# Performance work log

Measured on AMD Instinct MI355X. Metric: run time of the kernel, lower is better.

Reference implementation:

```python
import jax, jax.numpy as jnp
import numpy as np

NEG_SLOPE = 0.01  # nn.LeakyReLU default
EPS = 1e-5        # nn.LayerNorm default


def _layernorm(x):
    # parameter-free LayerNorm over last dim (source calls nn.LayerNorm() with no shape)
    mu = jnp.mean(x, axis=-1, keepdims=True)
    var = jnp.var(x, axis=-1, keepdims=True)
    return (x - mu) * jax.lax.rsqrt(var + EPS)


def _leaky_relu(x):
    return jnp.where(x >= 0, x, NEG_SLOPE * x)


def setup_inputs() -> dict:
    key = jax.random.key(0)
    ks = jax.random.split(key, 9)
    B, N, F_IN, F_HID, HEADS, F_OUT = 8, 1024, 384, 96, 8, 384
    s_v = 1.0 / np.sqrt(F_IN)
    s_qk = 1.0 / np.sqrt(F_HID)
    s_m = 1.0 / np.sqrt(F_HID * HEADS + F_IN)
    return {
        "X": jax.random.normal(ks[0], (B, N, F_IN), jnp.float32),
        "Wv": jax.random.uniform(ks[1], (F_IN, F_HID), jnp.float32, -s_v, s_v),
        "bv": jax.random.uniform(ks[2], (F_HID,), jnp.float32, -s_v, s_v),
        "Wq": jax.random.uniform(ks[3], (F_HID, HEADS), jnp.float32, -s_qk, s_qk),
        "bq": jax.random.uniform(ks[4], (HEADS,), jnp.float32, -s_qk, s_qk),
        "Wk": jax.random.uniform(ks[5], (F_HID, HEADS), jnp.float32, -s_qk, s_qk),
        "bk": jax.random.uniform(ks[6], (HEADS,), jnp.float32, -s_qk, s_qk),
        "Wm": jax.random.uniform(ks[7], (F_HID * HEADS + F_IN, F_OUT), jnp.float32, -s_m, s_m),
        "bm": jax.random.uniform(ks[8], (F_OUT,), jnp.float32, -s_m, s_m),
    }


def reference(X, Wv, bv, Wq, bq, Wk, bk, Wm, bm):
    B, N, _ = X.shape
    Hn = _layernorm(X)
    # MultiHeadGraphAtten
    V = Hn @ Wv + bv                      # [B, N, f_hid]
    Q = V @ Wq + bq                       # [B, N, heads]
    K = V @ Wk + bk                       # [B, N, heads]
    A = _leaky_relu(jnp.einsum('bih,bjh->bijh', Q, K))  # [B, N, N, heads]
    A = jax.nn.softmax(A, axis=3)         # softmax over heads (dim=3), faithful to source
    Hh = jnp.einsum('bijh,bjf->bihf', A, V)  # [B, N, heads, f_hid]
    H = Hh.reshape(B, N, -1)              # [B, N, heads*f_hid]
    H = jnp.concatenate([H, X], axis=2)   # residual concat
    O = _layernorm(H) @ Wm + bm
    O = _leaky_relu(O)                    # dropout is identity in eval
    return jnp.concatenate([O, H], axis=2)
```

## Files before the change

kernel.cpp:

```cpp
#include <hip/hip_runtime.h>
#include <hip/hip_bf16.h>
#include <math.h>

#define BB 8
#define NN 1024
#define F_IN 384
#define F_HID 96
#define HEADS 8
#define F_OUT 384
#define ROWS (BB*NN)
#define H_DIM 1152
#define OUT_DIM 1536
#define NEG 0.01f
#define LN_EPS 1e-5f
#define LOG2E 1.4426950408889634f

typedef __bf16 bf16x8 __attribute__((ext_vector_type(8)));
typedef float  f32x4  __attribute__((ext_vector_type(4)));

static __device__ __forceinline__ unsigned short b16u(float x) {
    union { __bf16 h; unsigned short u; } c; c.h = (__bf16)x; return c.u;
}
static __device__ __forceinline__ unsigned int pk2(float lo, float hi) {
    return (unsigned int)b16u(lo) | ((unsigned int)b16u(hi) << 16);
}

typedef __attribute__((address_space(1))) const unsigned char g1_t;
typedef __attribute__((address_space(3))) unsigned char l3_t;
static __device__ __forceinline__ void gl16(const void* g, void* l) {
    __builtin_amdgcn_global_load_lds((g1_t*)g, (l3_t*)l, 16, 0, 0);
}

__global__ __launch_bounds__(256) void kW(const float* __restrict__ Wm,
                                          const float* __restrict__ Wv,
                                          unsigned short* __restrict__ WmT,
                                          unsigned short* __restrict__ WvT) {
    __shared__ float tile[32][33];
    const int t = threadIdx.x;
    const int bid = (int)blockIdx.x;
    const float* src; unsigned short* dst;
    int k0, n0, srcld, dstld;
    if (bid < 432) {
        k0 = (bid / 12) * 32; n0 = (bid % 12) * 32;
        src = Wm; dst = WmT; srcld = F_OUT; dstld = H_DIM;
    } else {
        const int e = bid - 432;
        k0 = (e / 3) * 32; n0 = (e % 3) * 32;
        src = Wv; dst = WvT; srcld = F_HID; dstld = F_IN;
    }
#pragma unroll
    for (int p = 0; p < 4; ++p) {
        const int e = t + 256*p, kk = e >> 5, nn = e & 31;
        tile[kk][nn] = src[(size_t)(k0 + kk) * srcld + n0 + nn];
    }
    __syncthreads();
#pragma unroll
    for (int p = 0; p < 4; ++p) {
        const int e = t + 256*p, nn = e >> 5, kk = e & 31;
        dst[(size_t)(n0 + nn) * dstld + k0 + kk] = b16u(tile[kk][nn]);
    }
}

__global__ __launch_bounds__(384) void kA(const float* __restrict__ X,
                                          const unsigned short* __restrict__ WvT,
                                          const float* __restrict__ bv,
                                          const float* __restrict__ Wq, const float* __restrict__ bq,
                                          const float* __restrict__ Wk, const float* __restrict__ bk,
                                          unsigned short* __restrict__ VT,
                                          float* __restrict__ Qw, float* __restrict__ Kw) {
    __shared__ __align__(16) unsigned short xn[16][392];
    __shared__ float vsh[96][17];
    const int t = threadIdx.x;
    const int bid = (int)blockIdx.x;
    const int swz = (bid & 7) * 64 + (bid >> 3);
    const int i0 = swz * 16;
    const int b = i0 >> 10, i_in = i0 & 1023;
    const int w = t >> 6, l = t & 63, m = l & 15, g = l >> 4;

    if (t < 256) {
        const int r = t >> 4, l16 = t & 15;
        const float4* xrow = (const float4*)(X + (size_t)(i0 + r) * F_IN);
        float4 xv[6];
        float s = 0.f, sq = 0.f;
#pragma unroll
        for (int k = 0; k < 6; ++k) {
            xv[k] = xrow[l16 + 16*k];
            s  += xv[k].x + xv[k].y + xv[k].z + xv[k].w;
            sq += xv[k].x*xv[k].x + xv[k].y*xv[k].y + xv[k].z*xv[k].z + xv[k].w*xv[k].w;
        }
#pragma unroll
        for (int msk = 1; msk < 16; msk <<= 1) { s += __shfl_xor(s, msk); sq += __shfl_xor(sq, msk); }
        const float mu  = s * (1.f/F_IN);
        const float var = sq * (1.f/F_IN) - mu*mu;
        const float rstd = rsqrtf(var + LN_EPS);
#pragma unroll
        for (int k = 0; k < 6; ++k) {
            ushort4 h4;
            h4.x = b16u((xv[k].x - mu) * rstd);
            h4.y = b16u((xv[k].y - mu) * rstd);
            h4.z = b16u((xv[k].z - mu) * rstd);
            h4.w = b16u((xv[k].w - mu) * rstd);
            *(ushort4*)&xn[r][4*(l16 + 16*k)] = h4;
        }
    }
    __syncthreads();

    const f32x4 z4 = {0.f, 0.f, 0.f, 0.f};
    f32x4 acc = z4;
    const unsigned short* Br = WvT + (size_t)(w*16 + m) * F_IN + g*8;
#pragma unroll
    for (int ks = 0; ks < 12; ++ks) {
        const bf16x8 af  = *(const bf16x8*)&xn[m][ks*32 + g*8];
        const bf16x8 bfr = *(const bf16x8*)(Br + ks*32);
        acc = __builtin_amdgcn_mfma_f32_16x16x32_bf16(af, bfr, acc, 0, 0, 0);
    }
    {
        const int f = w*16 + m;
        const float bvv = bv[f];
#pragma unroll
        for (int r = 0; r < 4; ++r)
            vsh[f][g*4 + r] = acc[r] + bvv;
    }
    __syncthreads();

    {
        const int f = t >> 2, ic = (t & 3) * 4;
        ushort4 h4;
        h4.x = b16u(vsh[f][ic]);   h4.y = b16u(vsh[f][ic+1]);
        h4.z = b16u(vsh[f][ic+2]); h4.w = b16u(vsh[f][ic+3]);
        *(ushort4*)&VT[((size_t)b * F_HID + f) * NN + i_in + ic] = h4;
    }

    if (t < 256) {
        const int i_loc = t & 15, h = (t >> 4) & 7;
        const bool isQ = (t < 128);
        const float* Wx = isQ ? Wq : Wk;
        float a = isQ ? bq[h] : bk[h];
#pragma unroll 8
        for (int f = 0; f < F_HID; ++f)
            a = fmaf(vsh[f][i_loc], Wx[f*HEADS + h], a);
        if (isQ) Qw[(size_t)(i0 + i_loc) * HEADS + h] = a;
        else     Kw[(size_t)(i0 + i_loc) * HEADS + h] = a;
    }
}

__global__ __launch_bounds__(512, 4) void kB(const float* __restrict__ X,
                                             const unsigned short* __restrict__ VT,
                                             const float* __restrict__ Qw,
                                             const float* __restrict__ Kw,
                                             float* __restrict__ out,
                                             unsigned short* __restrict__ Hn) {
    __shared__ float q_sh[16][8];
    __shared__ float kT[2][HEADS][64];
    __shared__ __align__(16) unsigned short Wt[2][HEADS][16][64];
    __shared__ __align__(16) unsigned short vt_sh[2][F_HID][64];
    __shared__ float lnS[8][16], lnQ2[8][16];
    __shared__ float sxS[16], sx2S[16];
    __shared__ float mu_sh[16], rs_sh[16];

    const int t = threadIdx.x;
    const int bid = (int)blockIdx.x;
    const int swz = (bid & 7) * 64 + (bid >> 3);
    const int b  = swz >> 6;
    const int i0 = (swz & 63) * 16;
    const int w = t >> 6, l = t & 63, m = l & 15, g = l >> 4;
    const int hp = w >> 1, fh = w & 1;
    const int si = t >> 5, jd = t & 31;

    if (t < 128) ((float*)q_sh)[t] = Qw[((size_t)(b*NN + i0)) * HEADS + t];

    const f32x4 z4 = {0.f, 0.f, 0.f, 0.f};
    f32x4 acc[2][3];
#pragma unroll
    for (int h2 = 0; h2 < 2; ++h2)
#pragma unroll
        for (int fb = 0; fb < 3; ++fb) acc[h2][fb] = z4;

    const size_t vtbase = (size_t)b * F_HID * NN;
    const size_t krow   = (size_t)b * NN;

#define SMAX(kb, db)                                                                   \
    {                                                                                  \
        float2 kk[8];                                                                  \
        _Pragma("unroll")                                                              \
        for (int h = 0; h < 8; ++h)                                                    \
            kk[h] = *(const float2*)&kT[kb][h][2*jd];                                  \
        float p0[8], p1[8];                                                            \
        float s0 = 0.f, s1 = 0.f;                                                      \
        _Pragma("unroll")                                                              \
        for (int h = 0; h < 8; ++h) {                                                  \
            float a0 = q[h] * kk[h].x; a0 = fmaxf(a0, NEG*a0);                         \
            float a1 = q[h] * kk[h].y; a1 = fmaxf(a1, NEG*a1);                         \
            p0[h] = __builtin_amdgcn_exp2f(a0); s0 += p0[h];                           \
            p1[h] = __builtin_amdgcn_exp2f(a1); s1 += p1[h];                           \
        }                                                                              \
        const float inv0 = 1.f / s0, inv1 = 1.f / s1;                                  \
        char* wbase = (char*)Wt + (db)*16384 + si*128                                  \
                    + ((((jd>>2) ^ (si & 7))) << 4) + ((jd & 3) << 2);                 \
        _Pragma("unroll")                                                              \
        for (int h = 0; h < 8; ++h)                                                    \
            *(unsigned int*)(wbase + h*2048) = pk2(p0[h]*inv0, p1[h]*inv1);            \
    }

    {
        uint4 vr0, vr1;
        {
            const int f = t >> 3, u = t & 7;
            vr0 = *(const uint4*)(VT + vtbase + (size_t)f*NN + u*8);
        }
        if (t < 256) {
            const int e = t + 512, f2 = e >> 3, u2 = e & 7;
            vr1 = *(const uint4*)(VT + vtbase + (size_t)f2*NN + u2*8);
        }
        const float ka = Kw[(krow + l) * HEADS + w];
        const float kb_ = Kw[(krow + 64 + l) * HEADS + w];
        {
            const int f = t >> 3, u = t & 7;
            *(uint4*)((char*)vt_sh + f*128 + ((u ^ (f & 7)) << 4)) = vr0;
        }
        if (t < 256) {
            const int e = t + 512, f2 = e >> 3, u2 = e & 7;
            *(uint4*)((char*)vt_sh + f2*128 + ((u2 ^ (f2 & 7)) << 4)) = vr1;
        }
        kT[0][w][l] = ka;
        kT[1][w][l] = kb_;
    }
    __syncthreads();

    float q[8];
#pragma unroll
    for (int h = 0; h < 8; ++h) q[h] = q_sh[si][h] * LOG2E;

    SMAX(0, 0);
    __syncthreads();

    for (int c = 0; c < 16; ++c) {
        const int cur = c & 1, nxt = cur ^ 1;

        uint4 vr0, vr1; float kr = 0.f;
        if (c < 15) {
            const int j0n = (c + 1) * 64;
            {
                const int f = t >> 3, u = t & 7;
                vr0 = *(const uint4*)(VT + vtbase + (size_t)f*NN + j0n + u*8);
            }
            if (t < 256) {
                const int e = t + 512, f2 = e >> 3, u2 = e & 7;
                vr1 = *(const uint4*)(VT + vtbase + (size_t)f2*NN + j0n + u2*8);
            }
        }
        if (c < 14) kr = Kw[(krow + (size_t)(c + 2)*64 + l) * HEADS + w];

        if (c < 15) SMAX(nxt, nxt);

#pragma unroll
        for (int kh = 0; kh < 2; ++kh) {
            const int swzu = ((kh*4 + g) ^ (m & 7)) << 4;
            bf16x8 af[2];
#pragma unroll
            for (int h2 = 0; h2 < 2; ++h2)
                af[h2] = *(const bf16x8*)((const char*)Wt + cur*16384
                                          + (hp*2 + h2)*2048 + m*128 + swzu);
            bf16x8 bfr[3];
#pragma unroll
            for (int fb = 0; fb < 3; ++fb)
                bfr[fb] = *(const bf16x8*)((const char*)vt_sh + cur*12288
                                           + (fh*48 + fb*16 + m)*128 + swzu);
#pragma unroll
            for (int h2 = 0; h2 < 2; ++h2)
#pragma unroll
                for (int fb = 0; fb < 3; ++fb)
                    acc[h2][fb] = __builtin_amdgcn_mfma_f32_16x16x32_bf16(
                        af[h2], bfr[fb], acc[h2][fb], 0, 0, 0);
        }

        if (c < 15) {
            {
                const int f = t >> 3, u = t & 7;
                *(uint4*)((char*)vt_sh + nxt*12288 + f*128 + ((u ^ (f & 7)) << 4)) = vr0;
            }
            if (t < 256) {
                const int e = t + 512, f2 = e >> 3, u2 = e & 7;
                *(uint4*)((char*)vt_sh + nxt*12288 + f2*128 + ((u2 ^ (f2 & 7)) << 4)) = vr1;
            }
        }
        if (c < 14) kT[cur][w][l] = kr;
        __syncthreads();
    }
#undef SMAX

    float s[4] = {0,0,0,0}, s2[4] = {0,0,0,0};
#pragma unroll
    for (int h2 = 0; h2 < 2; ++h2)
#pragma unroll
        for (int fb = 0; fb < 3; ++fb)
#pragma unroll
            for (int r = 0; r < 4; ++r) {
                const float v = acc[h2][fb][r];
                s[r] += v; s2[r] += v*v;
            }
#pragma unroll
    for (int msk = 1; msk < 16; msk <<= 1)
#pragma unroll
        for (int r = 0; r < 4; ++r) {
            s[r]  += __shfl_xor(s[r],  msk);
            s2[r] += __shfl_xor(s2[r], msk);
        }
    if (m == 0) {
#pragma unroll
        for (int r = 0; r < 4; ++r) { lnS[w][g*4+r] = s[r]; lnQ2[w][g*4+r] = s2[r]; }
    }

    const int rX = t >> 5, lX = t & 31;
    const size_t xrow = (size_t)(b*NN + i0 + rX);
    const float4* x4 = (const float4*)(X + xrow * F_IN);
    float4 xs[3];
    float sx = 0.f, sx2 = 0.f;
#pragma unroll
    for (int kk = 0; kk < 3; ++kk) {
        xs[kk] = x4[lX + 32*kk];
        sx  += xs[kk].x + xs[kk].y + xs[kk].z + xs[kk].w;
        sx2 += xs[kk].x*xs[kk].x + xs[kk].y*xs[kk].y + xs[kk].z*xs[kk].z + xs[kk].w*xs[kk].w;
    }
#pragma unroll
    for (int msk = 1; msk < 32; msk <<= 1) { sx += __shfl_xor(sx, msk); sx2 += __shfl_xor(sx2, msk); }
    if (lX == 0) { sxS[rX] = sx; sx2S[rX] = sx2; }
    __syncthreads();

    if (t < 16) {
        float tot = sxS[t], tot2 = sx2S[t];
#pragma unroll
        for (int ww = 0; ww < 8; ++ww) { tot += lnS[ww][t]; tot2 += lnQ2[ww][t]; }
        const float muh = tot * (1.f/H_DIM);
        const float varh = tot2 * (1.f/H_DIM) - muh*muh;
        mu_sh[t] = muh; rs_sh[t] = rsqrtf(varh + LN_EPS);
    }
    __syncthreads();

#pragma unroll
    for (int r = 0; r < 4; ++r) {
        const int row = g*4 + r;
        const size_t orow = (size_t)(b*NN + i0 + row);
        const float muh = mu_sh[row], rs = rs_sh[row];
#pragma unroll
        for (int h2 = 0; h2 < 2; ++h2)
#pragma unroll
            for (int fb = 0; fb < 3; ++fb) {
                const int col = (hp*2 + h2)*F_HID + fh*48 + fb*16 + m;
                const float v = acc[h2][fb][r];
                out[orow * OUT_DIM + F_OUT + col] = v;
                Hn[orow * H_DIM + col] = b16u((v - muh) * rs);
            }
    }
    {
        const float muh = mu_sh[rX], rs = rs_sh[rX];
        float4* oX = (float4*)(out + xrow * OUT_DIM + F_OUT + HEADS*F_HID);
#pragma unroll
        for (int kk = 0; kk < 3; ++kk) {
            oX[lX + 32*kk] = xs[kk];
            ushort4 hh;
            hh.x = b16u((xs[kk].x - muh) * rs);
            hh.y = b16u((xs[kk].y - muh) * rs);
            hh.z = b16u((xs[kk].z - muh) * rs);
            hh.w = b16u((xs[kk].w - muh) * rs);
            *(ushort4*)&Hn[xrow * H_DIM + HEADS*F_HID + 4*(lX + 32*kk)] = hh;
        }
    }
}

__global__ __launch_bounds__(256) void kC(const unsigned short* __restrict__ Hn,
                                          const unsigned short* __restrict__ WmT,
                                          const float* __restrict__ bm,
                                          float* __restrict__ out) {
    __shared__ __align__(16) unsigned short As[2][64*64];
    __shared__ __align__(16) unsigned short Bs[2][48*64];
    const int t = threadIdx.x, w = t >> 6, lane = t & 63, m = lane & 15, g = lane >> 4;
    const int bid = (int)blockIdx.x;
    const int swz = (bid & 7) * 128 + (bid >> 3);
    const int i0 = (swz >> 3) * 64;
    const int n0 = (swz & 7) * 48;

    const f32x4 z4 = {0.f, 0.f, 0.f, 0.f};
    f32x4 acc[3];
#pragma unroll
    for (int ns = 0; ns < 3; ++ns) acc[ns] = z4;

#define KC_STAGE(buf, k0)                                                              \
    {                                                                                  \
        _Pragma("unroll")                                                              \
        for (int p = 0; p < 2; ++p) {                                                  \
            const int e = t + 256*p, row = e >> 3, c16 = e & 7;                        \
            gl16(Hn + (size_t)(i0+row)*H_DIM + (k0) + ((c16 ^ (row&7)) << 3),          \
                 (char*)As[buf] + e*16);                                               \
        }                                                                              \
        {                                                                              \
            const int row = t >> 3, c16 = t & 7;                                       \
            gl16(WmT + (size_t)(n0+row)*H_DIM + (k0) + ((c16 ^ (row&7)) << 3),         \
                 (char*)Bs[buf] + t*16);                                               \
        }                                                                              \
        if (t < 128) {                                                                 \
            const int e = t + 256, row = e >> 3, c16 = e & 7;                          \
            gl16(WmT + (size_t)(n0+row)*H_DIM + (k0) + ((c16 ^ (row&7)) << 3),         \
                 (char*)Bs[buf] + e*16);                                               \
        }                                                                              \
    }

    KC_STAGE(0, 0);
    __syncthreads();

    for (int s = 0; s < 18; ++s) {
        const int cur = s & 1;
        if (s < 17) KC_STAGE(cur ^ 1, (s + 1) * 64);
#pragma unroll
        for (int kh = 0; kh < 2; ++kh) {
            const int kb = kh*64 + g*16;
            const int rowA = w*16 + m;
            const bf16x8 af = *(const bf16x8*)((const char*)As[cur] + rowA*128
                                               + (kb ^ ((rowA&7)<<4)));
#pragma unroll
            for (int ns = 0; ns < 3; ++ns) {
                const int row = ns*16 + m;
                const bf16x8 bf_ = *(const bf16x8*)((const char*)Bs[cur] + row*128
                                                    + (kb ^ ((row&7)<<4)));
                acc[ns] = __builtin_amdgcn_mfma_f32_16x16x32_bf16(af, bf_, acc[ns], 0, 0, 0);
            }
        }
        __syncthreads();
    }
#undef KC_STAGE

#pragma unroll
    for (int ns = 0; ns < 3; ++ns) {
        const int col = n0 + ns*16 + m;
        const float bmv = bm[col];
#pragma unroll
        for (int r = 0; r < 4; ++r) {
            float o = acc[ns][r] + bmv;
            o = fmaxf(o, NEG * o);
            out[(size_t)(i0 + w*16 + g*4 + r) * OUT_DIM + col] = o;
        }
    }
}

extern "C" void kernel_launch(void* const* d_in, const int* in_sizes, int n_in,
                              void* d_out, int out_size, void* d_ws, size_t ws_size,
                              hipStream_t stream) {
    const float* X  = (const float*)d_in[0];
    const float* Wv = (const float*)d_in[1];
    const float* bv = (const float*)d_in[2];
    const float* Wq = (const float*)d_in[3];
    const float* bq = (const float*)d_in[4];
    const float* Wk = (const float*)d_in[5];
    const float* bk = (const float*)d_in[6];
    const float* Wm = (const float*)d_in[7];
    const float* bm = (const float*)d_in[8];
    float* out = (float*)d_out;

    char* p = (char*)d_ws;
    unsigned short* VT  = (unsigned short*)p;                 p += (size_t)BB*F_HID*NN*2;
    float*          Qw  = (float*)p;                          p += (size_t)ROWS*HEADS*4;
    float*          Kw  = (float*)p;                          p += (size_t)ROWS*HEADS*4;
    unsigned short* WmT = (unsigned short*)p;                 p += (size_t)F_OUT*H_DIM*2;
    unsigned short* WvT = (unsigned short*)p;                 p += (size_t)F_HID*F_IN*2;
    unsigned short* Hn  = (unsigned short*)p;
    (void)ws_size; (void)out_size; (void)n_in; (void)in_sizes;

    kW<<<468, 256, 0, stream>>>(Wm, Wv, WmT, WvT);
    kA<<<ROWS/16, 384, 0, stream>>>(X, WvT, bv, Wq, bq, Wk, bk, VT, Qw, Kw);
    kB<<<BB*(NN/16), 512, 0, stream>>>(X, VT, Qw, Kw, out, Hn);
    kC<<<(ROWS/64)*(F_OUT/48), 256, 0, stream>>>(Hn, WmT, bm, out);
}
```

Before: 72.39 us.

## Double kB block to 1024 threads with warp-specialized loaders and split-K MFMA

```diff
diff --git a/kernel.cpp b/kernel.cpp
--- a/kernel.cpp
+++ b/kernel.cpp
@@ -144,19 +144,21 @@
     }
 }
 
-__global__ __launch_bounds__(512, 4) void kB(const float* __restrict__ X,
-                                             const unsigned short* __restrict__ VT,
-                                             const float* __restrict__ Qw,
-                                             const float* __restrict__ Kw,
-                                             float* __restrict__ out,
-                                             unsigned short* __restrict__ Hn) {
-    __shared__ float q_sh[16][8];
-    __shared__ float kT[2][HEADS][64];
-    __shared__ __align__(16) unsigned short Wt[2][HEADS][16][64];
-    __shared__ __align__(16) unsigned short vt_sh[2][F_HID][64];
-    __shared__ float lnS[8][16], lnQ2[8][16];
-    __shared__ float sxS[16], sx2S[16];
-    __shared__ float mu_sh[16], rs_sh[16];
+__global__ __launch_bounds__(1024, 8) void kB(const float* __restrict__ X,
+                                              const unsigned short* __restrict__ VT,
+                                              const float* __restrict__ Qw,
+                                              const float* __restrict__ Kw,
+                                              float* __restrict__ out,
+                                              unsigned short* __restrict__ Hn) {
+    __shared__ __align__(16) char L[63232];
+    float* KT  = (float*)(L + 57344);
+    float* QS  = (float*)(L + 61440);
+    float* LNS = (float*)(L + 61952);
+    float* LNQ = (float*)(L + 62464);
+    float* SXS = (float*)(L + 62976);
+    float* SX2 = (float*)(L + 63040);
+    float* MU  = (float*)(L + 63104);
+    float* RS  = (float*)(L + 63168);
 
     const int t = threadIdx.x;
     const int bid = (int)blockIdx.x;
@@ -164,10 +166,9 @@
     const int b  = swz >> 6;
     const int i0 = (swz & 63) * 16;
     const int w = t >> 6, l = t & 63, m = l & 15, g = l >> 4;
-    const int hp = w >> 1, fh = w & 1;
-    const int si = t >> 5, jd = t & 31;
-
-    if (t < 128) ((float*)q_sh)[t] = Qw[((size_t)(b*NN + i0)) * HEADS + t];
+    const int hp = w >> 2, fh = (w >> 1) & 1, jh = w & 1;
+    const int si = (t >> 5) & 15, jd = t & 31;
+    const int ts = t - 512;
 
     const f32x4 z4 = {0.f, 0.f, 0.f, 0.f};
     f32x4 acc[2][3];
@@ -184,7 +185,7 @@
         float2 kk[8];                                                                  \
         _Pragma("unroll")                                                              \
         for (int h = 0; h < 8; ++h)                                                    \
-            kk[h] = *(const float2*)&kT[kb][h][2*jd];                                  \
+            kk[h] = *(const float2*)&KT[(kb)*512 + h*64 + 2*jd];                       \
         float p0[8], p1[8];                                                            \
         float s0 = 0.f, s1 = 0.f;                                                      \
         _Pragma("unroll")                                                              \
@@ -195,77 +196,79 @@
             p1[h] = __builtin_amdgcn_exp2f(a1); s1 += p1[h];                           \
         }                                                                              \
         const float inv0 = 1.f / s0, inv1 = 1.f / s1;                                  \
-        char* wbase = (char*)Wt + (db)*16384 + si*128                                  \
+        char* wbase = L + (db)*16384 + si*128                                          \
                     + ((((jd>>2) ^ (si & 7))) << 4) + ((jd & 3) << 2);                 \
         _Pragma("unroll")                                                              \
         for (int h = 0; h < 8; ++h)                                                    \
             *(unsigned int*)(wbase + h*2048) = pk2(p0[h]*inv0, p1[h]*inv1);            \
     }
 
-    {
+    if (t >= 512) {
         uint4 vr0, vr1;
         {
-            const int f = t >> 3, u = t & 7;
+            const int f = ts >> 3, u = ts & 7;
             vr0 = *(const uint4*)(VT + vtbase + (size_t)f*NN + u*8);
         }
-        if (t < 256) {
-            const int e = t + 512, f2 = e >> 3, u2 = e & 7;
+        if (ts < 256) {
+            const int e = ts + 512, f2 = e >> 3, u2 = e & 7;
             vr1 = *(const uint4*)(VT + vtbase + (size_t)f2*NN + u2*8);
         }
-        const float ka = Kw[(krow + l) * HEADS + w];
-        const float kb_ = Kw[(krow + 64 + l) * HEADS + w];
+        const float ka = Kw[(krow + (ts & 63)) * HEADS + (ts >> 6)];
+        const float kb_ = Kw[(krow + 64 + (ts & 63)) * HEADS + (ts >> 6)];
         {
-            const int f = t >> 3, u = t & 7;
-            *(uint4*)((char*)vt_sh + f*128 + ((u ^ (f & 7)) << 4)) = vr0;
-        }
-        if (t < 256) {
-            const int e = t + 512, f2 = e >> 3, u2 = e & 7;
-            *(uint4*)((char*)vt_sh + f2*128 + ((u2 ^ (f2 & 7)) << 4)) = vr1;
-        }
-        kT[0][w][l] = ka;
-        kT[1][w][l] = kb_;
-    }
+            const int f = ts >> 3, u = ts & 7;
+            *(uint4*)(L + 32768 + f*128 + ((u ^ (f & 7)) << 4)) = vr0;
+        }
+        if (ts < 256) {
+            const int e = ts + 512, f2 = e >> 3, u2 = e & 7;
+            *(uint4*)(L + 32768 + f2*128 + ((u2 ^ (f2 & 7)) << 4)) = vr1;
+        }
+        KT[0*512 + (ts >> 6)*64 + (ts & 63)] = ka;
+        KT[1*512 + (ts >> 6)*64 + (ts & 63)] = kb_;
+    }
+    if (t < 128) QS[t] = Qw[((size_t)(b*NN + i0)) * HEADS + t];
     __syncthreads();
 
     float q[8];
 #pragma unroll
-    for (int h = 0; h < 8; ++h) q[h] = q_sh[si][h] * LOG2E;
-
-    SMAX(0, 0);
+    for (int h = 0; h < 8; ++h) q[h] = QS[si*8 + h] * LOG2E;
+
+    if (t < 512) SMAX(0, 0);
     __syncthreads();
 
     for (int c = 0; c < 16; ++c) {
         const int cur = c & 1, nxt = cur ^ 1;
 
         uint4 vr0, vr1; float kr = 0.f;
-        if (c < 15) {
-            const int j0n = (c + 1) * 64;
-            {
-                const int f = t >> 3, u = t & 7;
-                vr0 = *(const uint4*)(VT + vtbase + (size_t)f*NN + j0n + u*8);
+        if (t >= 512) {
+            if (c < 15) {
+                const int j0n = (c + 1) * 64;
+                {
+                    const int f = ts >> 3, u = ts & 7;
+                    vr0 = *(const uint4*)(VT + vtbase + (size_t)f*NN + j0n + u*8);
+                }
+                if (ts < 256) {
+                    const int e = ts + 512, f2 = e >> 3, u2 = e & 7;
+                    vr1 = *(const uint4*)(VT + vtbase + (size_t)f2*NN + j0n + u2*8);
+                }
             }
-            if (t < 256) {
-                const int e = t + 512, f2 = e >> 3, u2 = e & 7;
-                vr1 = *(const uint4*)(VT + vtbase + (size_t)f2*NN + j0n + u2*8);
+            if (c < 14) kr = Kw[(krow + (size_t)(c + 2)*64 + (ts & 63)) * HEADS + (ts >> 6)];
+        }
+
+        if (t < 512 && c < 15) SMAX(nxt, nxt);
+
+        {
+            const int swzu = (((jh << 2) | g) ^ (m & 7)) << 4;
+            bf16x8 af[2];
+#pragma unroll
+            for (int h2 = 0; h2 < 2; ++h2)
+                af[h2] = *(const bf16x8*)(L + cur*16384 + (hp*2 + h2)*2048 + m*128 + swzu);
+            bf16x8 bfr[3];
+#pragma unroll
+            for (int fb = 0; fb < 3; ++fb) {
+                const int f = fh*48 + fb*16 + m;
+                bfr[fb] = *(const bf16x8*)(L + 32768 + cur*12288 + f*128 + swzu);
             }
-        }
-        if (c < 14) kr = Kw[(krow + (size_t)(c + 2)*64 + l) * HEADS + w];
-
-        if (c < 15) SMAX(nxt, nxt);
-
-#pragma unroll
-        for (int kh = 0; kh < 2; ++kh) {
-            const int swzu = ((kh*4 + g) ^ (m & 7)) << 4;
-            bf16x8 af[2];
-#pragma unroll
-            for (int h2 = 0; h2 < 2; ++h2)
-                af[h2] = *(const bf16x8*)((const char*)Wt + cur*16384
-                                          + (hp*2 + h2)*2048 + m*128 + swzu);
-            bf16x8 bfr[3];
-#pragma unroll
-            for (int fb = 0; fb < 3; ++fb)
-                bfr[fb] = *(const bf16x8*)((const char*)vt_sh + cur*12288
-                                           + (fh*48 + fb*16 + m)*128 + swzu);
 #pragma unroll
             for (int h2 = 0; h2 < 2; ++h2)
 #pragma unroll
@@ -274,96 +277,127 @@
                         af[h2], bfr[fb], acc[h2][fb], 0, 0, 0);
         }
 
-        if (c < 15) {
-            {
-                const int f = t >> 3, u = t & 7;
-                *(uint4*)((char*)vt_sh + nxt*12288 + f*128 + ((u ^ (f & 7)) << 4)) = vr0;
+        if (t >= 512) {
+            if (c < 15) {
+                {
+                    const int f = ts >> 3, u = ts & 7;
+                    *(uint4*)(L + 32768 + nxt*12288 + f*128 + ((u ^ (f & 7)) << 4)) = vr0;
+                }
+                if (ts < 256) {
+                    const int e = ts + 512, f2 = e >> 3, u2 = e & 7;
+                    *(uint4*)(L + 32768 + nxt*12288 + f2*128 + ((u2 ^ (f2 & 7)) << 4)) = vr1;
+                }
             }
-            if (t < 256) {
-                const int e = t + 512, f2 = e >> 3, u2 = e & 7;
-                *(uint4*)((char*)vt_sh + nxt*12288 + f2*128 + ((u2 ^ (f2 & 7)) << 4)) = vr1;
+            if (c < 14) KT[cur*512 + (ts >> 6)*64 + (ts & 63)] = kr;
+        }
+        __syncthreads();
+    }
+#undef SMAX
+
+    float* SC = (float*)L;
+    const int r8 = hp*2 + fh;
+    if (jh == 1) {
+#pragma unroll
+        for (int h2 = 0; h2 < 2; ++h2)
+#pragma unroll
+            for (int fb = 0; fb < 3; ++fb)
+#pragma unroll
+                for (int r = 0; r < 4; ++r)
+                    SC[(r8*64 + l)*24 + h2*12 + fb*4 + r] = acc[h2][fb][r];
+    }
+    __syncthreads();
+    if (jh == 0) {
+#pragma unroll
+        for (int h2 = 0; h2 < 2; ++h2)
+#pragma unroll
+            for (int fb = 0; fb < 3; ++fb)
+#pragma unroll
+                for (int r = 0; r < 4; ++r)
+                    acc[h2][fb][r] += SC[(r8*64 + l)*24 + h2*12 + fb*4 + r];
+    }
+
+    const int tv = ((t >> 7) << 6) | l;
+    if (jh == 0) {
+        float s[4] = {0,0,0,0}, s2[4] = {0,0,0,0};
+#pragma unroll
+        for (int h2 = 0; h2 < 2; ++h2)
+#pragma unroll
+            for (int fb = 0; fb < 3; ++fb)
+#pragma unroll
+                for (int r = 0; r < 4; ++r) {
+                    const float v = acc[h2][fb][r];
+                    s[r] += v; s2[r] += v*v;
+                }
+#pragma unroll
+        for (int msk = 1; msk < 16; msk <<= 1)
+#pragma unroll
+            for (int r = 0; r < 4; ++r) {
+                s[r]  += __shfl_xor(s[r],  msk);
+                s2[r] += __shfl_xor(s2[r], msk);
             }
-        }
-        if (c < 14) kT[cur][w][l] = kr;
-        __syncthreads();
-    }
-#undef SMAX
-
-    float s[4] = {0,0,0,0}, s2[4] = {0,0,0,0};
-#pragma unroll
-    for (int h2 = 0; h2 < 2; ++h2)
-#pragma unroll
-        for (int fb = 0; fb < 3; ++fb)
-#pragma unroll
-            for (int r = 0; r < 4; ++r) {
-                const float v = acc[h2][fb][r];
-                s[r] += v; s2[r] += v*v;
-            }
-#pragma unroll
-    for (int msk = 1; msk < 16; msk <<= 1)
-#pragma unroll
-        for (int r = 0; r < 4; ++r) {
-            s[r]  += __shfl_xor(s[r],  msk);
-            s2[r] += __shfl_xor(s2[r], msk);
-        }
-    if (m == 0) {
-#pragma unroll
-        for (int r = 0; r < 4; ++r) { lnS[w][g*4+r] = s[r]; lnQ2[w][g*4+r] = s2[r]; }
-    }
-
-    const int rX = t >> 5, lX = t & 31;
+        if (m == 0) {
+#pragma unroll
+            for (int r = 0; r < 4; ++r) { LNS[r8*16 + g*4+r] = s[r]; LNQ[r8*16 + g*4+r] = s2[r]; }
+        }
+    }
+
+    const int rX = tv >> 5, lX = tv & 31;
     const size_t xrow = (size_t)(b*NN + i0 + rX);
-    const float4* x4 = (const float4*)(X + xrow * F_IN);
     float4 xs[3];
-    float sx = 0.f, sx2 = 0.f;
-#pragma unroll
-    for (int kk = 0; kk < 3; ++kk) {
-        xs[kk] = x4[lX + 32*kk];
-        sx  += xs[kk].x + xs[kk].y + xs[kk].z + xs[kk].w;
-        sx2 += xs[kk].x*xs[kk].x + xs[kk].y*xs[kk].y + xs[kk].z*xs[kk].z + xs[kk].w*xs[kk].w;
-    }
-#pragma unroll
-    for (int msk = 1; msk < 32; msk <<= 1) { sx += __shfl_xor(sx, msk); sx2 += __shfl_xor(sx2, msk); }
-    if (lX == 0) { sxS[rX] = sx; sx2S[rX] = sx2; }
+    if (jh == 0) {
+        const float4* x4 = (const float4*)(X + xrow * F_IN);
+        float sx = 0.f, sx2 = 0.f;
+#pragma unroll
+        for (int kk = 0; kk < 3; ++kk) {
+            xs[kk] = x4[lX + 32*kk];
+            sx  += xs[kk].x + xs[kk].y + xs[kk].z + xs[kk].w;
+            sx2 += xs[kk].x*xs[kk].x + xs[kk].y*xs[kk].y + xs[kk].z*xs[kk].z + xs[kk].w*xs[kk].w;
+        }
+#pragma unroll
+        for (int msk = 1; msk < 32; msk <<= 1) { sx += __shfl_xor(sx, msk); sx2 += __shfl_xor(sx2, msk); }
+        if (lX == 0) { SXS[rX] = sx; SX2[rX] = sx2; }
+    }
     __syncthreads();
 
     if (t < 16) {
-        float tot = sxS[t], tot2 = sx2S[t];
-#pragma unroll
-        for (int ww = 0; ww < 8; ++ww) { tot += lnS[ww][t]; tot2 += lnQ2[ww][t]; }
+        float tot = SXS[t], tot2 = SX2[t];
+#pragma unroll
+        for (int ww = 0; ww < 8; ++ww) { tot += LNS[ww*16 + t]; tot2 += LNQ[ww*16 + t]; }
         const float muh = tot * (1.f/H_DIM);
         const float varh = tot2 * (1.f/H_DIM) - muh*muh;
-        mu_sh[t] = muh; rs_sh[t] = rsqrtf(varh + LN_EPS);
-    }
-    __syncthreads();
-
-#pragma unroll
-    for (int r = 0; r < 4; ++r) {
-        const int row = g*4 + r;
-        const size_t orow = (size_t)(b*NN + i0 + row);
-        const float muh = mu_sh[row], rs = rs_sh[row];
-#pragma unroll
-        for (int h2 = 0; h2 < 2; ++h2)
-#pragma unroll
-            for (int fb = 0; fb < 3; ++fb) {
-                const int col = (hp*2 + h2)*F_HID + fh*48 + fb*16 + m;
-                const float v = acc[h2][fb][r];
-                out[orow * OUT_DIM + F_OUT + col] = v;
-                Hn[orow * H_DIM + col] = b16u((v - muh) * rs);
+        MU[t] = muh; RS[t] = rsqrtf(varh + LN_EPS);
+    }
+    __syncthreads();
+
+    if (jh == 0) {
+#pragma unroll
+        for (int r = 0; r < 4; ++r) {
+            const int row = g*4 + r;
+            const size_t orow = (size_t)(b*NN + i0 + row);
+            const float muh = MU[row], rs = RS[row];
+#pragma unroll
+            for (int h2 = 0; h2 < 2; ++h2)
+#pragma unroll
+                for (int fb = 0; fb < 3; ++fb) {
+                    const int col = (hp*2 + h2)*F_HID + fh*48 + fb*16 + m;
+                    const float v = acc[h2][fb][r];
+                    out[orow * OUT_DIM + F_OUT + col] = v;
+                    Hn[orow * H_DIM + col] = b16u((v - muh) * rs);
+                }
+        }
+        {
+            const float muh = MU[rX], rs = RS[rX];
+            float4* oX = (float4*)(out + xrow * OUT_DIM + F_OUT + HEADS*F_HID);
+#pragma unroll
+            for (int kk = 0; kk < 3; ++kk) {
+                oX[lX + 32*kk] = xs[kk];
+                ushort4 hh;
+                hh.x = b16u((xs[kk].x - muh) * rs);
+                hh.y = b16u((xs[kk].y - muh) * rs);
+                hh.z = b16u((xs[kk].z - muh) * rs);
+                hh.w = b16u((xs[kk].w - muh) * rs);
+                *(ushort4*)&Hn[xrow * H_DIM + HEADS*F_HID + 4*(lX + 32*kk)] = hh;
             }
-    }
-    {
-        const float muh = mu_sh[rX], rs = rs_sh[rX];
-        float4* oX = (float4*)(out + xrow * OUT_DIM + F_OUT + HEADS*F_HID);
-#pragma unroll
-        for (int kk = 0; kk < 3; ++kk) {
-            oX[lX + 32*kk] = xs[kk];
-            ushort4 hh;
-            hh.x = b16u((xs[kk].x - muh) * rs);
-            hh.y = b16u((xs[kk].y - muh) * rs);
-            hh.z = b16u((xs[kk].z - muh) * rs);
-            hh.w = b16u((xs[kk].w - muh) * rs);
-            *(ushort4*)&Hn[xrow * H_DIM + HEADS*F_HID + 4*(lX + 32*kk)] = hh;
         }
     }
 }
@@ -467,6 +501,6 @@
 
     kW<<<468, 256, 0, stream>>>(Wm, Wv, WmT, WvT);
     kA<<<ROWS/16, 384, 0, stream>>>(X, WvT, bv, Wq, bq, Wk, bk, VT, Qw, Kw);
-    kB<<<BB*(NN/16), 512, 0, stream>>>(X, VT, Qw, Kw, out, Hn);
+    kB<<<BB*(NN/16), 1024, 0, stream>>>(X, VT, Qw, Kw, out, Hn);
     kC<<<(ROWS/64)*(F_OUT/48), 256, 0, stream>>>(Hn, WmT, bm, out);
 }
```

After: 92.09 us. 1.27x slower.

## Fuse output projection GEMM into attention kernel, keeping normalized H in LDS

Applied to the files above, without the earlier changes.

```diff
diff --git a/kernel.cpp b/kernel.cpp
--- a/kernel.cpp
+++ b/kernel.cpp
@@ -148,15 +148,18 @@
                                              const unsigned short* __restrict__ VT,
                                              const float* __restrict__ Qw,
                                              const float* __restrict__ Kw,
-                                             float* __restrict__ out,
-                                             unsigned short* __restrict__ Hn) {
-    __shared__ float q_sh[16][8];
-    __shared__ float kT[2][HEADS][64];
-    __shared__ __align__(16) unsigned short Wt[2][HEADS][16][64];
-    __shared__ __align__(16) unsigned short vt_sh[2][F_HID][64];
-    __shared__ float lnS[8][16], lnQ2[8][16];
-    __shared__ float sxS[16], sx2S[16];
-    __shared__ float mu_sh[16], rs_sh[16];
+                                             const unsigned short* __restrict__ WmT,
+                                             const float* __restrict__ bm,
+                                             float* __restrict__ out) {
+    __shared__ __align__(16) char L[63232];
+    float* KT  = (float*)(L + 57344);
+    float* QS  = (float*)(L + 61440);
+    float* LNS = (float*)(L + 61952);
+    float* LNQ = (float*)(L + 62464);
+    float* SXS = (float*)(L + 62976);
+    float* SX2 = (float*)(L + 63040);
+    float* MU  = (float*)(L + 63104);
+    float* RS  = (float*)(L + 63168);
 
     const int t = threadIdx.x;
     const int bid = (int)blockIdx.x;
@@ -167,8 +170,6 @@
     const int hp = w >> 1, fh = w & 1;
     const int si = t >> 5, jd = t & 31;
 
-    if (t < 128) ((float*)q_sh)[t] = Qw[((size_t)(b*NN + i0)) * HEADS + t];
-
     const f32x4 z4 = {0.f, 0.f, 0.f, 0.f};
     f32x4 acc[2][3];
 #pragma unroll
@@ -184,7 +185,7 @@
         float2 kk[8];                                                                  \
         _Pragma("unroll")                                                              \
         for (int h = 0; h < 8; ++h)                                                    \
-            kk[h] = *(const float2*)&kT[kb][h][2*jd];                                  \
+            kk[h] = *(const float2*)&KT[(kb)*512 + h*64 + 2*jd];                       \
         float p0[8], p1[8];                                                            \
         float s0 = 0.f, s1 = 0.f;                                                      \
         _Pragma("unroll")                                                              \
@@ -195,7 +196,7 @@
             p1[h] = __builtin_amdgcn_exp2f(a1); s1 += p1[h];                           \
         }                                                                              \
         const float inv0 = 1.f / s0, inv1 = 1.f / s1;                                  \
-        char* wbase = (char*)Wt + (db)*16384 + si*128                                  \
+        char* wbase = L + (db)*16384 + si*128                                          \
                     + ((((jd>>2) ^ (si & 7))) << 4) + ((jd & 3) << 2);                 \
         _Pragma("unroll")                                                              \
         for (int h = 0; h < 8; ++h)                                                    \
@@ -216,20 +217,21 @@
         const float kb_ = Kw[(krow + 64 + l) * HEADS + w];
         {
             const int f = t >> 3, u = t & 7;
-            *(uint4*)((char*)vt_sh + f*128 + ((u ^ (f & 7)) << 4)) = vr0;
+            *(uint4*)(L + 32768 + f*128 + ((u ^ (f & 7)) << 4)) = vr0;
         }
         if (t < 256) {
             const int e = t + 512, f2 = e >> 3, u2 = e & 7;
-            *(uint4*)((char*)vt_sh + f2*128 + ((u2 ^ (f2 & 7)) << 4)) = vr1;
-        }
-        kT[0][w][l] = ka;
-        kT[1][w][l] = kb_;
-    }
+            *(uint4*)(L + 32768 + f2*128 + ((u2 ^ (f2 & 7)) << 4)) = vr1;
+        }
+        KT[0*512 + w*64 + l] = ka;
+        KT[1*512 + w*64 + l] = kb_;
+    }
+    if (t < 128) QS[t] = Qw[((size_t)(b*NN + i0)) * HEADS + t];
     __syncthreads();
 
     float q[8];
 #pragma unroll
-    for (int h = 0; h < 8; ++h) q[h] = q_sh[si][h] * LOG2E;
+    for (int h = 0; h < 8; ++h) q[h] = QS[si*8 + h] * LOG2E;
 
     SMAX(0, 0);
     __syncthreads();
@@ -259,13 +261,13 @@
             bf16x8 af[2];
 #pragma unroll
             for (int h2 = 0; h2 < 2; ++h2)
-                af[h2] = *(const bf16x8*)((const char*)Wt + cur*16384
-                                          + (hp*2 + h2)*2048 + m*128 + swzu);
+                af[h2] = *(const bf16x8*)(L + cur*16384 + (hp*2 + h2)*2048 + m*128 + swzu);
             bf16x8 bfr[3];
 #pragma unroll
-            for (int fb = 0; fb < 3; ++fb)
-                bfr[fb] = *(const bf16x8*)((const char*)vt_sh + cur*12288
-                                           + (fh*48 + fb*16 + m)*128 + swzu);
+            for (int fb = 0; fb < 3; ++fb) {
+                const int f = fh*48 + fb*16 + m;
+                bfr[fb] = *(const bf16x8*)(L + 32768 + cur*12288 + f*128 + swzu);
+            }
 #pragma unroll
             for (int h2 = 0; h2 < 2; ++h2)
 #pragma unroll
@@ -277,14 +279,14 @@
         if (c < 15) {
             {
                 const int f = t >> 3, u = t & 7;
-                *(uint4*)((char*)vt_sh + nxt*12288 + f*128 + ((u ^ (f & 7)) << 4)) = vr0;
+                *(uint4*)(L + 32768 + nxt*12288 + f*128 + ((u ^ (f & 7)) << 4)) = vr0;
             }
             if (t < 256) {
                 const int e = t + 512, f2 = e >> 3, u2 = e & 7;
-                *(uint4*)((char*)vt_sh + nxt*12288 + f2*128 + ((u2 ^ (f2 & 7)) << 4)) = vr1;
-            }
-        }
-        if (c < 14) kT[cur][w][l] = kr;
+                *(uint4*)(L + 32768 + nxt*12288 + f2*128 + ((u2 ^ (f2 & 7)) << 4)) = vr1;
+            }
+        }
+        if (c < 14) KT[cur*512 + w*64 + l] = kr;
         __syncthreads();
     }
 #undef SMAX
@@ -308,7 +310,7 @@
         }
     if (m == 0) {
 #pragma unroll
-        for (int r = 0; r < 4; ++r) { lnS[w][g*4+r] = s[r]; lnQ2[w][g*4+r] = s2[r]; }
+        for (int r = 0; r < 4; ++r) { LNS[w*16 + g*4+r] = s[r]; LNQ[w*16 + g*4+r] = s2[r]; }
     }
 
     const int rX = t >> 5, lX = t & 31;
@@ -324,24 +326,25 @@
     }
 #pragma unroll
     for (int msk = 1; msk < 32; msk <<= 1) { sx += __shfl_xor(sx, msk); sx2 += __shfl_xor(sx2, msk); }
-    if (lX == 0) { sxS[rX] = sx; sx2S[rX] = sx2; }
+    if (lX == 0) { SXS[rX] = sx; SX2[rX] = sx2; }
     __syncthreads();
 
     if (t < 16) {
-        float tot = sxS[t], tot2 = sx2S[t];
-#pragma unroll
-        for (int ww = 0; ww < 8; ++ww) { tot += lnS[ww][t]; tot2 += lnQ2[ww][t]; }
+        float tot = SXS[t], tot2 = SX2[t];
+#pragma unroll
+        for (int ww = 0; ww < 8; ++ww) { tot += LNS[ww*16 + t]; tot2 += LNQ[ww*16 + t]; }
         const float muh = tot * (1.f/H_DIM);
         const float varh = tot2 * (1.f/H_DIM) - muh*muh;
-        mu_sh[t] = muh; rs_sh[t] = rsqrtf(varh + LN_EPS);
-    }
-    __syncthreads();
-
+        MU[t] = muh; RS[t] = rsqrtf(varh + LN_EPS);
+    }
+    __syncthreads();
+
+    unsigned short* HL = (unsigned short*)L;
 #pragma unroll
     for (int r = 0; r < 4; ++r) {
         const int row = g*4 + r;
         const size_t orow = (size_t)(b*NN + i0 + row);
-        const float muh = mu_sh[row], rs = rs_sh[row];
+        const float muh = MU[row], rs = RS[row];
 #pragma unroll
         for (int h2 = 0; h2 < 2; ++h2)
 #pragma unroll
@@ -349,11 +352,11 @@
                 const int col = (hp*2 + h2)*F_HID + fh*48 + fb*16 + m;
                 const float v = acc[h2][fb][r];
                 out[orow * OUT_DIM + F_OUT + col] = v;
-                Hn[orow * H_DIM + col] = b16u((v - muh) * rs);
+                HL[row*1160 + col] = b16u((v - muh) * rs);
             }
     }
     {
-        const float muh = mu_sh[rX], rs = rs_sh[rX];
+        const float muh = MU[rX], rs = RS[rX];
         float4* oX = (float4*)(out + xrow * OUT_DIM + F_OUT + HEADS*F_HID);
 #pragma unroll
         for (int kk = 0; kk < 3; ++kk) {
@@ -363,81 +366,33 @@
             hh.y = b16u((xs[kk].y - muh) * rs);
             hh.z = b16u((xs[kk].z - muh) * rs);
             hh.w = b16u((xs[kk].w - muh) * rs);
-            *(ushort4*)&Hn[xrow * H_DIM + HEADS*F_HID + 4*(lX + 32*kk)] = hh;
-        }
-    }
-}
-
-__global__ __launch_bounds__(256) void kC(const unsigned short* __restrict__ Hn,
-                                          const unsigned short* __restrict__ WmT,
-                                          const float* __restrict__ bm,
-                                          float* __restrict__ out) {
-    __shared__ __align__(16) unsigned short As[2][64*64];
-    __shared__ __align__(16) unsigned short Bs[2][48*64];
-    const int t = threadIdx.x, w = t >> 6, lane = t & 63, m = lane & 15, g = lane >> 4;
-    const int bid = (int)blockIdx.x;
-    const int swz = (bid & 7) * 128 + (bid >> 3);
-    const int i0 = (swz >> 3) * 64;
-    const int n0 = (swz & 7) * 48;
-
-    const f32x4 z4 = {0.f, 0.f, 0.f, 0.f};
-    f32x4 acc[3];
-#pragma unroll
-    for (int ns = 0; ns < 3; ++ns) acc[ns] = z4;
-
-#define KC_STAGE(buf, k0)                                                              \
-    {                                                                                  \
-        _Pragma("unroll")                                                              \
-        for (int p = 0; p < 2; ++p) {                                                  \
-            const int e = t + 256*p, row = e >> 3, c16 = e & 7;                        \
-            gl16(Hn + (size_t)(i0+row)*H_DIM + (k0) + ((c16 ^ (row&7)) << 3),          \
-                 (char*)As[buf] + e*16);                                               \
-        }                                                                              \
-        {                                                                              \
-            const int row = t >> 3, c16 = t & 7;                                       \
-            gl16(WmT + (size_t)(n0+row)*H_DIM + (k0) + ((c16 ^ (row&7)) << 3),         \
-                 (char*)Bs[buf] + t*16);                                               \
-        }                                                                              \
-        if (t < 128) {                                                                 \
-            const int e = t + 256, row = e >> 3, c16 = e & 7;                          \
-            gl16(WmT + (size_t)(n0+row)*H_DIM + (k0) + ((c16 ^ (row&7)) << 3),         \
-                 (char*)Bs[buf] + e*16);                                               \
-        }                                                                              \
-    }
-
-    KC_STAGE(0, 0);
-    __syncthreads();
-
-    for (int s = 0; s < 18; ++s) {
-        const int cur = s & 1;
-        if (s < 17) KC_STAGE(cur ^ 1, (s + 1) * 64);
-#pragma unroll
-        for (int kh = 0; kh < 2; ++kh) {
-            const int kb = kh*64 + g*16;
-            const int rowA = w*16 + m;
-            const bf16x8 af = *(const bf16x8*)((const char*)As[cur] + rowA*128
-                                               + (kb ^ ((rowA&7)<<4)));
-#pragma unroll
-            for (int ns = 0; ns < 3; ++ns) {
-                const int row = ns*16 + m;
-                const bf16x8 bf_ = *(const bf16x8*)((const char*)Bs[cur] + row*128
-                                                    + (kb ^ ((row&7)<<4)));
-                acc[ns] = __builtin_amdgcn_mfma_f32_16x16x32_bf16(af, bf_, acc[ns], 0, 0, 0);
-            }
-        }
-        __syncthreads();
-    }
-#undef KC_STAGE
-
+            *(ushort4*)&HL[rX*1160 + HEADS*F_HID + 4*(lX + 32*kk)] = hh;
+        }
+    }
+    __syncthreads();
+
+    f32x4 oacc[3];
+#pragma unroll
+    for (int ns = 0; ns < 3; ++ns) oacc[ns] = z4;
+#pragma unroll 4
+    for (int ks = 0; ks < 36; ++ks) {
+        const bf16x8 af = *(const bf16x8*)((const char*)HL + m*2320 + ks*64 + g*16);
+#pragma unroll
+        for (int ns = 0; ns < 3; ++ns) {
+            const bf16x8 bfr = *(const bf16x8*)(WmT + (size_t)(w*48 + ns*16 + m)*H_DIM
+                                                + ks*32 + g*8);
+            oacc[ns] = __builtin_amdgcn_mfma_f32_16x16x32_bf16(af, bfr, oacc[ns], 0, 0, 0);
+        }
+    }
 #pragma unroll
     for (int ns = 0; ns < 3; ++ns) {
-        const int col = n0 + ns*16 + m;
+        const int col = w*48 + ns*16 + m;
         const float bmv = bm[col];
 #pragma unroll
         for (int r = 0; r < 4; ++r) {
-            float o = acc[ns][r] + bmv;
+            float o = oacc[ns][r] + bmv;
             o = fmaxf(o, NEG * o);
-            out[(size_t)(i0 + w*16 + g*4 + r) * OUT_DIM + col] = o;
+            out[(size_t)(b*NN + i0 + g*4 + r) * OUT_DIM + col] = o;
         }
     }
 }
@@ -462,11 +417,9 @@
     float*          Kw  = (float*)p;                          p += (size_t)ROWS*HEADS*4;
     unsigned short* WmT = (unsigned short*)p;                 p += (size_t)F_OUT*H_DIM*2;
     unsigned short* WvT = (unsigned short*)p;                 p += (size_t)F_HID*F_IN*2;
-    unsigned short* Hn  = (unsigned short*)p;
     (void)ws_size; (void)out_size; (void)n_in; (void)in_sizes;
 
     kW<<<468, 256, 0, stream>>>(Wm, Wv, WmT, WvT);
     kA<<<ROWS/16, 384, 0, stream>>>(X, WvT, bv, Wq, bq, Wk, bk, VT, Qw, Kw);
-    kB<<<BB*(NN/16), 512, 0, stream>>>(X, VT, Qw, Kw, out, Hn);
-    kC<<<(ROWS/64)*(F_OUT/48), 256, 0, stream>>>(Hn, WmT, bm, out);
-}
+    kB<<<BB*(NN/16), 512, 0, stream>>>(X, VT, Qw, Kw, WmT, bm, out);
+}
```

New measurement: 95.23 us. 31.6% more time.
